# Kernel tuning notes

Measured on AMD Instinct MI355X. Metric: run time of the kernel, lower is better.

## Reference

```python
import jax, jax.numpy as jnp
import numpy as np

D_PAIR, C, N_HEAD = 128, 32, 4
HC = N_HEAD * C

def setup_inputs() -> dict:
    key = jax.random.key(0)
    ks = jax.random.split(key, 8)
    B, N = 1, 384
    Z_raw = jax.random.normal(ks[0], (B, N, N, D_PAIR), dtype=jnp.float32)
    Z_mask = jnp.ones((B, N, N), dtype=jnp.float32)
    s = 1.0 / np.sqrt(D_PAIR)
    return {
        'Z_raw': Z_raw,
        'Z_mask': Z_mask,
        'ln_w': jnp.ones((D_PAIR,), jnp.float32),
        'ln_b': jnp.zeros((D_PAIR,), jnp.float32),
        'W_b': jax.random.uniform(ks[1], (D_PAIR, N_HEAD), jnp.float32, -s, s),
        'W_qkv': jax.random.uniform(ks[2], (D_PAIR, 3 * HC), jnp.float32, -s, s),
        'W_gate': jnp.zeros((D_PAIR, HC), jnp.float32),
        'gating_bias': jnp.ones((HC,), jnp.float32),
        'W_o': jnp.zeros((HC, D_PAIR), jnp.float32),
        'out_bias': jnp.zeros((D_PAIR,), jnp.float32),
    }

def reference(Z_raw, Z_mask, ln_w, ln_b, W_b, W_qkv, W_gate, gating_bias, W_o, out_bias):
    B, N, _, D = Z_raw.shape
    # LayerNorm over d_pair
    mu = jnp.mean(Z_raw, axis=-1, keepdims=True)
    var = jnp.var(Z_raw, axis=-1, keepdims=True)
    Z = (Z_raw - mu) * jax.lax.rsqrt(var + 1e-5) * ln_w + ln_b
    # nonbatched triangle bias: [B, h, q, k]
    bias = jnp.einsum('bqkh->bhqk', jnp.einsum('bqkd,dh->bqkh', Z, W_b))
    # qkv projection: [B, N(rows), N, 3*h*c]
    qkv = jnp.einsum('bind,de->bine', Z, W_qkv)
    q, k, v = jnp.split(qkv, 3, axis=-1)
    resh = lambda t: t.reshape(B, N, N, N_HEAD, C).transpose(0, 1, 3, 2, 4)  # [B,i,h,n,c]
    q, k, v = resh(q) * (C ** -0.5), resh(k), resh(v)
    logits = jnp.einsum('bihqc,bihkc->bihqk', q, k)
    mask_bias = (Z_mask - 1.0) * 1e9  # [B, i, k]
    logits = logits + mask_bias[:, :, None, None, :] + bias[:, None, :, :, :]
    weights = jax.nn.softmax(logits, axis=-1)
    wa = jnp.einsum('bihqk,bihkc->bihqc', weights, v)
    wa = wa.transpose(0, 1, 3, 2, 4).reshape(B, N, N, HC)
    gate = jax.nn.sigmoid(jnp.einsum('bind,de->bine', Z, W_gate) + gating_bias)
    out = jnp.einsum('bine,ed->bind', gate * wa, W_o)
    # bias_dropout_add with training=False -> plain bias + residual add
    return Z_raw + out + out_bias
```

## Files before the change

### kernel.cpp

```cpp
#include <hip/hip_runtime.h>
#include <hip/hip_bf16.h>

#define NN 384
#define DP 128
#define NHEAD 4
#define CH 32
#define HCC 128

typedef __hip_bfloat16 bf16;
typedef __bf16 bf16x8 __attribute__((ext_vector_type(8)));
typedef __bf16 bf16x4 __attribute__((ext_vector_type(4)));
typedef float floatx4 __attribute__((ext_vector_type(4)));

#define QKSTRIDE 40
#define VPSTRIDE 408
#define WSTRIDE 136

__device__ __forceinline__ float b2f(bf16 x){ return __bfloat162float(x); }
__device__ __forceinline__ bf16 f2b(float x){ return __float2bfloat16(x); }

__global__ __launch_bounds__(256) void wt_kernel(
    const float* __restrict__ Wqkv, __bf16* __restrict__ Wt)
{
  int idx = blockIdx.x * 256 + threadIdx.x;
  int d = idx / NN, col = idx - d * NN;
  Wt[col * DP + d] = (__bf16)Wqkv[idx];
}

__global__ __launch_bounds__(256) void wgo_kernel(
    const float* __restrict__ Wg, const float* __restrict__ Wo,
    __bf16* __restrict__ WgT, __bf16* __restrict__ WoT)
{
  int idx = blockIdx.x * 256 + threadIdx.x;
  int r = idx >> 7, c = idx & 127;
  WgT[idx] = (__bf16)Wg[c * 128 + r];
  WoT[idx] = (__bf16)Wo[c * 128 + r];
}

__global__ __launch_bounds__(256) void ln_bias_kernel(
    const float* __restrict__ Zr, const float* __restrict__ lnw,
    const float* __restrict__ lnb, const float* __restrict__ Wb,
    bf16* __restrict__ Zn, float* __restrict__ bias)
{
  int t = threadIdx.x;
  int grp = t >> 5, lane32 = t & 31;
  int pos = blockIdx.x * 8 + grp;
  size_t base = (size_t)pos * DP;
  const float4 x = *(const float4*)(Zr + base + lane32 * 4);
  float s  = x.x + x.y + x.z + x.w;
  float s2 = x.x*x.x + x.y*x.y + x.z*x.z + x.w*x.w;
  #pragma unroll
  for (int m = 1; m < 32; m <<= 1){ s += __shfl_xor(s, m); s2 += __shfl_xor(s2, m); }
  float mean = s * (1.0f / DP);
  float var  = s2 * (1.0f / DP) - mean * mean;
  float rstd = rsqrtf(var + 1e-5f);
  const float4 w4 = *(const float4*)(lnw + lane32 * 4);
  const float4 b4 = *(const float4*)(lnb + lane32 * 4);
  float z0 = (x.x - mean) * rstd * w4.x + b4.x;
  float z1 = (x.y - mean) * rstd * w4.y + b4.y;
  float z2 = (x.z - mean) * rstd * w4.z + b4.z;
  float z3 = (x.w - mean) * rstd * w4.w + b4.w;
  bf16x4 zb = { (__bf16)z0, (__bf16)z1, (__bf16)z2, (__bf16)z3 };
  *(bf16x4*)((__bf16*)Zn + base + lane32 * 4) = zb;
  const float4 wb0 = *(const float4*)(Wb + (lane32 * 4 + 0) * NHEAD);
  const float4 wb1 = *(const float4*)(Wb + (lane32 * 4 + 1) * NHEAD);
  const float4 wb2 = *(const float4*)(Wb + (lane32 * 4 + 2) * NHEAD);
  const float4 wb3 = *(const float4*)(Wb + (lane32 * 4 + 3) * NHEAD);
  float p0 = z0*wb0.x + z1*wb1.x + z2*wb2.x + z3*wb3.x;
  float p1 = z0*wb0.y + z1*wb1.y + z2*wb2.y + z3*wb3.y;
  float p2 = z0*wb0.z + z1*wb1.z + z2*wb2.z + z3*wb3.z;
  float p3 = z0*wb0.w + z1*wb1.w + z2*wb2.w + z3*wb3.w;
  #pragma unroll
  for (int m = 1; m < 32; m <<= 1){
    p0 += __shfl_xor(p0, m); p1 += __shfl_xor(p1, m);
    p2 += __shfl_xor(p2, m); p3 += __shfl_xor(p3, m);
  }
  if (lane32 == 0){
    bias[0 * NN * NN + pos] = p0;
    bias[1 * NN * NN + pos] = p1;
    bias[2 * NN * NN + pos] = p2;
    bias[3 * NN * NN + pos] = p3;
  }
}

__global__ __launch_bounds__(256, 1) void attn_kernel(
    const __bf16* __restrict__ Zn, const __bf16* __restrict__ Wt,
    const float* __restrict__ Zm, const float* __restrict__ bias,
    __bf16* __restrict__ wa)
{
  __shared__ __align__(16) __bf16 qs[NN * QKSTRIDE];
  __shared__ __align__(16) __bf16 ks[NN * QKSTRIDE];
  __shared__ __align__(16) __bf16 vs[CH * VPSTRIDE];
  __shared__ __align__(16) __bf16 ps[4 * 16 * VPSTRIDE];
  __shared__ float maskb[NN];

  int i = blockIdx.x >> 2;
  int h = blockIdx.x & 3;
  int t = threadIdx.x;
  int wv = t >> 6;
  int lane = t & 63;
  int m16 = lane & 15;
  int quad = lane >> 4;

  for (int k = t; k < NN; k += 256)
    maskb[k] = (Zm[(size_t)i * NN + k] - 1.0f) * 1e9f;

  const float qscale = 0.17677669529663687f;

  for (int mt = wv * 6; mt < wv * 6 + 6; mt++){
    bf16x8 afr[4];
    const __bf16* arow = Zn + (size_t)(i * NN + mt * 16 + m16) * DP + quad * 8;
    #pragma unroll
    for (int kc = 0; kc < 4; kc++) afr[kc] = *(const bf16x8*)(arow + kc * 32);
    for (int nt = 0; nt < 6; nt++){
      int mat = nt >> 1;
      int colbase = mat * HCC + h * CH + (nt & 1) * 16;
      const __bf16* brow = Wt + (size_t)(colbase + m16) * DP + quad * 8;
      floatx4 acc = {0.f, 0.f, 0.f, 0.f};
      #pragma unroll
      for (int kc = 0; kc < 4; kc++){
        bf16x8 bfr = *(const bf16x8*)(brow + kc * 32);
        acc = __builtin_amdgcn_mfma_f32_16x16x32_bf16(afr[kc], bfr, acc, 0, 0, 0);
      }
      int ccol = (nt & 1) * 16 + m16;
      #pragma unroll
      for (int reg = 0; reg < 4; reg++){
        int row = mt * 16 + quad * 4 + reg;
        float v = acc[reg];
        if (mat == 0)      qs[row * QKSTRIDE + ccol] = (__bf16)(v * qscale);
        else if (mat == 1) ks[row * QKSTRIDE + ccol] = (__bf16)v;
        else               vs[ccol * VPSTRIDE + row] = (__bf16)v;
      }
    }
  }
  __syncthreads();

  const float* brow_base = bias + (size_t)h * NN * NN;
  __bf16* pw = ps + wv * 16 * VPSTRIDE;

  for (int s = 0; s < 6; s++){
    int strip = wv * 6 + s;
    bf16x8 qf = *(const bf16x8*)(qs + (strip * 16 + m16) * QKSTRIDE + quad * 8);
    floatx4 sacc[24];
    #pragma unroll
    for (int kt = 0; kt < 24; kt++){
      bf16x8 kf = *(const bf16x8*)(ks + (kt * 16 + m16) * QKSTRIDE + quad * 8);
      floatx4 z = {0.f, 0.f, 0.f, 0.f};
      sacc[kt] = __builtin_amdgcn_mfma_f32_16x16x32_bf16(qf, kf, z, 0, 0, 0);
    }
    float mx[4] = {-1e30f, -1e30f, -1e30f, -1e30f};
    #pragma unroll
    for (int kt = 0; kt < 24; kt++){
      int col = kt * 16 + m16;
      float mb = maskb[col];
      #pragma unroll
      for (int reg = 0; reg < 4; reg++){
        int row = strip * 16 + quad * 4 + reg;
        float v = sacc[kt][reg] + brow_base[(size_t)row * NN + col] + mb;
        sacc[kt][reg] = v;
        mx[reg] = fmaxf(mx[reg], v);
      }
    }
    #pragma unroll
    for (int reg = 0; reg < 4; reg++)
      for (int msk = 1; msk < 16; msk <<= 1)
        mx[reg] = fmaxf(mx[reg], __shfl_xor(mx[reg], msk));
    float sm[4] = {0.f, 0.f, 0.f, 0.f};
    #pragma unroll
    for (int kt = 0; kt < 24; kt++){
      int col = kt * 16 + m16;
      #pragma unroll
      for (int reg = 0; reg < 4; reg++){
        float p = __expf(sacc[kt][reg] - mx[reg]);
        sm[reg] += p;
        pw[(quad * 4 + reg) * VPSTRIDE + col] = (__bf16)p;
      }
    }
    #pragma unroll
    for (int reg = 0; reg < 4; reg++)
      for (int msk = 1; msk < 16; msk <<= 1)
        sm[reg] += __shfl_xor(sm[reg], msk);
    float inv[4];
    #pragma unroll
    for (int reg = 0; reg < 4; reg++) inv[reg] = 1.0f / sm[reg];

    floatx4 oacc[2] = {{0.f,0.f,0.f,0.f},{0.f,0.f,0.f,0.f}};
    #pragma unroll
    for (int kc = 0; kc < 12; kc++){
      bf16x8 pa = *(const bf16x8*)(pw + m16 * VPSTRIDE + kc * 32 + quad * 8);
      #pragma unroll
      for (int ct = 0; ct < 2; ct++){
        bf16x8 vb = *(const bf16x8*)(vs + (ct * 16 + m16) * VPSTRIDE + kc * 32 + quad * 8);
        oacc[ct] = __builtin_amdgcn_mfma_f32_16x16x32_bf16(pa, vb, oacc[ct], 0, 0, 0);
      }
    }
    #pragma unroll
    for (int ct = 0; ct < 2; ct++){
      #pragma unroll
      for (int reg = 0; reg < 4; reg++){
        int row = strip * 16 + quad * 4 + reg;
        wa[(size_t)(i * NN + row) * HCC + h * CH + ct * 16 + m16] =
            (__bf16)(oacc[ct][reg] * inv[reg]);
      }
    }
  }
}

__global__ __launch_bounds__(256, 1) void out_kernel(
    const float* __restrict__ Zr, const __bf16* __restrict__ Zn,
    const __bf16* __restrict__ wa, const __bf16* __restrict__ WgT,
    const float* __restrict__ gb, const __bf16* __restrict__ WoT,
    const float* __restrict__ ob, float* __restrict__ out)
{
  __shared__ __align__(16) __bf16 wgs[128 * WSTRIDE];
  __shared__ __align__(16) __bf16 wos[128 * WSTRIDE];
  __shared__ __align__(16) __bf16 gsh[4][16 * WSTRIDE];
  __shared__ float gbs[HCC], obs[DP];

  int t = threadIdx.x;
  int wv = t >> 6, lane = t & 63;
  int m16 = lane & 15, quad = lane >> 4;

  for (int idx = t * 8; idx < 128 * 128; idx += 256 * 8){
    int r = idx >> 7, c = idx & 127;
    *(bf16x8*)(wgs + r * WSTRIDE + c) = *(const bf16x8*)(WgT + idx);
    *(bf16x8*)(wos + r * WSTRIDE + c) = *(const bf16x8*)(WoT + idx);
  }
  if (t < 128){ gbs[t] = gb[t]; obs[t] = ob[t]; }
  __syncthreads();

  int mbase = blockIdx.x * 128;
  __bf16* gstrip = gsh[wv];

  for (int sp = 0; sp < 2; sp++){
    int row0 = mbase + (sp * 4 + wv) * 16;
    bf16x8 afr[4];
    const __bf16* arow = Zn + (size_t)(row0 + m16) * DP + quad * 8;
    #pragma unroll
    for (int kc = 0; kc < 4; kc++) afr[kc] = *(const bf16x8*)(arow + kc * 32);
    #pragma unroll
    for (int nt = 0; nt < 8; nt++){
      floatx4 acc = {0.f, 0.f, 0.f, 0.f};
      #pragma unroll
      for (int kc = 0; kc < 4; kc++){
        bf16x8 bfr = *(const bf16x8*)(wgs + (nt * 16 + m16) * WSTRIDE + kc * 32 + quad * 8);
        acc = __builtin_amdgcn_mfma_f32_16x16x32_bf16(afr[kc], bfr, acc, 0, 0, 0);
      }
      int col = nt * 16 + m16;
      #pragma unroll
      for (int reg = 0; reg < 4; reg++){
        int row = row0 + quad * 4 + reg;
        float g = 1.0f / (1.0f + __expf(-(acc[reg] + gbs[col])));
        float w = __bfloat162float(wa[(size_t)row * HCC + col]);
        gstrip[(quad * 4 + reg) * WSTRIDE + col] = (__bf16)(g * w);
      }
    }
    bf16x8 gfr[4];
    #pragma unroll
    for (int kc = 0; kc < 4; kc++)
      gfr[kc] = *(const bf16x8*)(gstrip + m16 * WSTRIDE + kc * 32 + quad * 8);
    #pragma unroll
    for (int nt = 0; nt < 8; nt++){
      floatx4 acc = {0.f, 0.f, 0.f, 0.f};
      #pragma unroll
      for (int kc = 0; kc < 4; kc++){
        bf16x8 bfr = *(const bf16x8*)(wos + (nt * 16 + m16) * WSTRIDE + kc * 32 + quad * 8);
        acc = __builtin_amdgcn_mfma_f32_16x16x32_bf16(gfr[kc], bfr, acc, 0, 0, 0);
      }
      int col = nt * 16 + m16;
      #pragma unroll
      for (int reg = 0; reg < 4; reg++){
        int row = row0 + quad * 4 + reg;
        size_t off = (size_t)row * DP + col;
        out[off] = Zr[off] + acc[reg] + obs[col];
      }
    }
  }
}

extern "C" void kernel_launch(void* const* d_in, const int* in_sizes, int n_in,
                              void* d_out, int out_size, void* d_ws, size_t ws_size,
                              hipStream_t stream)
{
  const float* Zr   = (const float*)d_in[0];
  const float* Zm   = (const float*)d_in[1];
  const float* lnw  = (const float*)d_in[2];
  const float* lnb  = (const float*)d_in[3];
  const float* Wb   = (const float*)d_in[4];
  const float* Wqkv = (const float*)d_in[5];
  const float* Wg   = (const float*)d_in[6];
  const float* gb   = (const float*)d_in[7];
  const float* Wo   = (const float*)d_in[8];
  const float* ob   = (const float*)d_in[9];
  float* out = (float*)d_out;

  char* ws = (char*)d_ws;
  size_t off = 0;
  bf16*   Zn   = (bf16*)(ws + off);           off += (size_t)NN * NN * DP * 2;
  float*  bias = (float*)(ws + off);          off += (size_t)NHEAD * NN * NN * 4;
  bf16*   wa   = (bf16*)(ws + off);           off += (size_t)NN * NN * HCC * 2;
  __bf16* Wt   = (__bf16*)(ws + off);         off += (size_t)3 * HCC * DP * 2;
  __bf16* WgT  = (__bf16*)(ws + off);         off += (size_t)DP * HCC * 2;
  __bf16* WoT  = (__bf16*)(ws + off);         off += (size_t)HCC * DP * 2;

  wt_kernel<<<(3 * HCC * DP) / 256, 256, 0, stream>>>(Wqkv, Wt);
  wgo_kernel<<<(DP * HCC) / 256, 256, 0, stream>>>(Wg, Wo, WgT, WoT);
  ln_bias_kernel<<<NN * NN / 8, 256, 0, stream>>>(Zr, lnw, lnb, Wb, Zn, bias);
  attn_kernel<<<NN * NHEAD, 256, 0, stream>>>((const __bf16*)Zn, Wt, Zm, bias, (__bf16*)wa);
  out_kernel<<<NN * NN / 128, 256, 0, stream>>>(Zr, (const __bf16*)Zn, (const __bf16*)wa,
                                                WgT, gb, WoT, ob, out);
}
```

Baseline: 493.5 us.

## Split QKV projection into a separate GEMM kernel and stream Q/K/V from global

Moves the per-row QKV projection out of the attention kernel into a dedicated qkv_gemm kernel. That kernel loads Z once per row-block for all heads and writes Q, K and a transposed V to global workspace. The query scale is folded into the weight transpose. The attention kernel now reads Q/K/V from global, seeds the MFMA accumulator with bias plus mask, and uses a transposed MFMA layout for lane-local softmax reductions and vectorized stores. It drops the large Q/K/V shared buffers to allow two blocks per CU, at the cost of extra global traffic for the Q/K/V intermediates.

```diff
diff --git a/kernel.cpp b/kernel.cpp
--- a/kernel.cpp
+++ b/kernel.cpp
@@ -12,9 +12,8 @@
 typedef __bf16 bf16x4 __attribute__((ext_vector_type(4)));
 typedef float floatx4 __attribute__((ext_vector_type(4)));
 
-#define QKSTRIDE 40
-#define VPSTRIDE 408
 #define WSTRIDE 136
+#define PSTR 392
 
 __device__ __forceinline__ float b2f(bf16 x){ return __bfloat162float(x); }
 __device__ __forceinline__ bf16 f2b(float x){ return __float2bfloat16(x); }
@@ -22,9 +21,12 @@
 __global__ __launch_bounds__(256) void wt_kernel(
     const float* __restrict__ Wqkv, __bf16* __restrict__ Wt)
 {
+  const float qscale = 0.17677669529663687f;
   int idx = blockIdx.x * 256 + threadIdx.x;
   int d = idx / NN, col = idx - d * NN;
-  Wt[col * DP + d] = (__bf16)Wqkv[idx];
+  float v = Wqkv[idx];
+  if (col < HCC) v *= qscale;
+  Wt[col * DP + d] = (__bf16)v;
 }
 
 __global__ __launch_bounds__(256) void wgo_kernel(
@@ -83,125 +85,129 @@
   }
 }
 
-__global__ __launch_bounds__(256, 1) void attn_kernel(
+__global__ __launch_bounds__(256) void qkv_gemm(
     const __bf16* __restrict__ Zn, const __bf16* __restrict__ Wt,
-    const float* __restrict__ Zm, const float* __restrict__ bias,
-    __bf16* __restrict__ wa)
-{
-  __shared__ __align__(16) __bf16 qs[NN * QKSTRIDE];
-  __shared__ __align__(16) __bf16 ks[NN * QKSTRIDE];
-  __shared__ __align__(16) __bf16 vs[CH * VPSTRIDE];
-  __shared__ __align__(16) __bf16 ps[4 * 16 * VPSTRIDE];
-  __shared__ float maskb[NN];
+    __bf16* __restrict__ q_g, __bf16* __restrict__ k_g, __bf16* __restrict__ v_g)
+{
+  int i = blockIdx.x >> 1;
+  int half = blockIdx.x & 1;
+  int t = threadIdx.x;
+  int wv = t >> 6, lane = t & 63;
+  int m16 = lane & 15, quad = lane >> 4;
+
+  int mrow0 = half * 192 + wv * 48;
+
+  bf16x8 zf[3][4];
+  #pragma unroll
+  for (int mt = 0; mt < 3; mt++){
+    const __bf16* zrow = Zn + (size_t)(i * NN + mrow0 + mt * 16 + m16) * DP + quad * 8;
+    #pragma unroll
+    for (int kc = 0; kc < 4; kc++) zf[mt][kc] = *(const bf16x8*)(zrow + kc * 32);
+  }
+
+  for (int nt = 0; nt < 24; nt++){
+    bf16x8 wf[4];
+    const __bf16* wrow = Wt + (size_t)(nt * 16 + m16) * DP + quad * 8;
+    #pragma unroll
+    for (int kc = 0; kc < 4; kc++) wf[kc] = *(const bf16x8*)(wrow + kc * 32);
+    #pragma unroll
+    for (int mt = 0; mt < 3; mt++){
+      floatx4 acc = {0.f, 0.f, 0.f, 0.f};
+      if (nt < 16){
+        #pragma unroll
+        for (int kc = 0; kc < 4; kc++)
+          acc = __builtin_amdgcn_mfma_f32_16x16x32_bf16(wf[kc], zf[mt][kc], acc, 0, 0, 0);
+        bf16x4 pk = { (__bf16)acc[0], (__bf16)acc[1], (__bf16)acc[2], (__bf16)acc[3] };
+        int row = i * NN + mrow0 + mt * 16 + m16;
+        if (nt < 8)
+          *(bf16x4*)(q_g + (size_t)row * HCC + nt * 16 + quad * 4) = pk;
+        else
+          *(bf16x4*)(k_g + (size_t)row * HCC + (nt - 8) * 16 + quad * 4) = pk;
+      } else {
+        #pragma unroll
+        for (int kc = 0; kc < 4; kc++)
+          acc = __builtin_amdgcn_mfma_f32_16x16x32_bf16(zf[mt][kc], wf[kc], acc, 0, 0, 0);
+        bf16x4 pk = { (__bf16)acc[0], (__bf16)acc[1], (__bf16)acc[2], (__bf16)acc[3] };
+        int c = (nt - 16) * 16 + m16;
+        *(bf16x4*)(v_g + ((size_t)i * HCC + c) * NN + mrow0 + mt * 16 + quad * 4) = pk;
+      }
+    }
+  }
+}
+
+__global__ __launch_bounds__(256, 2) void attn_kernel(
+    const __bf16* __restrict__ q_g, const __bf16* __restrict__ k_g,
+    const __bf16* __restrict__ v_g, const float* __restrict__ Zm,
+    const float* __restrict__ bias, __bf16* __restrict__ wa)
+{
+  __shared__ __align__(16) __bf16 ps[4 * 16 * PSTR];
+  __shared__ __align__(16) float maskb[NN];
 
   int i = blockIdx.x >> 2;
   int h = blockIdx.x & 3;
   int t = threadIdx.x;
-  int wv = t >> 6;
-  int lane = t & 63;
-  int m16 = lane & 15;
-  int quad = lane >> 4;
+  int wv = t >> 6, lane = t & 63;
+  int m16 = lane & 15, quad = lane >> 4;
 
   for (int k = t; k < NN; k += 256)
     maskb[k] = (Zm[(size_t)i * NN + k] - 1.0f) * 1e9f;
-
-  const float qscale = 0.17677669529663687f;
-
-  for (int mt = wv * 6; mt < wv * 6 + 6; mt++){
-    bf16x8 afr[4];
-    const __bf16* arow = Zn + (size_t)(i * NN + mt * 16 + m16) * DP + quad * 8;
-    #pragma unroll
-    for (int kc = 0; kc < 4; kc++) afr[kc] = *(const bf16x8*)(arow + kc * 32);
-    for (int nt = 0; nt < 6; nt++){
-      int mat = nt >> 1;
-      int colbase = mat * HCC + h * CH + (nt & 1) * 16;
-      const __bf16* brow = Wt + (size_t)(colbase + m16) * DP + quad * 8;
-      floatx4 acc = {0.f, 0.f, 0.f, 0.f};
-      #pragma unroll
-      for (int kc = 0; kc < 4; kc++){
-        bf16x8 bfr = *(const bf16x8*)(brow + kc * 32);
-        acc = __builtin_amdgcn_mfma_f32_16x16x32_bf16(afr[kc], bfr, acc, 0, 0, 0);
-      }
-      int ccol = (nt & 1) * 16 + m16;
-      #pragma unroll
-      for (int reg = 0; reg < 4; reg++){
-        int row = mt * 16 + quad * 4 + reg;
-        float v = acc[reg];
-        if (mat == 0)      qs[row * QKSTRIDE + ccol] = (__bf16)(v * qscale);
-        else if (mat == 1) ks[row * QKSTRIDE + ccol] = (__bf16)v;
-        else               vs[ccol * VPSTRIDE + row] = (__bf16)v;
-      }
-    }
-  }
   __syncthreads();
 
-  const float* brow_base = bias + (size_t)h * NN * NN;
-  __bf16* pw = ps + wv * 16 * VPSTRIDE;
+  __bf16* pw = ps + wv * 16 * PSTR;
+  const float* bh = bias + (size_t)h * NN * NN;
 
   for (int s = 0; s < 6; s++){
     int strip = wv * 6 + s;
-    bf16x8 qf = *(const bf16x8*)(qs + (strip * 16 + m16) * QKSTRIDE + quad * 8);
+    int qrow = strip * 16 + m16;
+    bf16x8 qf = *(const bf16x8*)(q_g + (size_t)(i * NN + qrow) * HCC + h * CH + quad * 8);
     floatx4 sacc[24];
     #pragma unroll
     for (int kt = 0; kt < 24; kt++){
-      bf16x8 kf = *(const bf16x8*)(ks + (kt * 16 + m16) * QKSTRIDE + quad * 8);
-      floatx4 z = {0.f, 0.f, 0.f, 0.f};
-      sacc[kt] = __builtin_amdgcn_mfma_f32_16x16x32_bf16(qf, kf, z, 0, 0, 0);
-    }
-    float mx[4] = {-1e30f, -1e30f, -1e30f, -1e30f};
+      int k0 = kt * 16 + quad * 4;
+      floatx4 cin = *(const floatx4*)(bh + (size_t)qrow * NN + k0);
+      floatx4 mk  = *(const floatx4*)(maskb + k0);
+      cin += mk;
+      bf16x8 kf = *(const bf16x8*)(k_g + (size_t)(i * NN + kt * 16 + m16) * HCC + h * CH + quad * 8);
+      sacc[kt] = __builtin_amdgcn_mfma_f32_16x16x32_bf16(kf, qf, cin, 0, 0, 0);
+    }
+    float mx = -1e30f;
     #pragma unroll
     for (int kt = 0; kt < 24; kt++){
-      int col = kt * 16 + m16;
-      float mb = maskb[col];
-      #pragma unroll
-      for (int reg = 0; reg < 4; reg++){
-        int row = strip * 16 + quad * 4 + reg;
-        float v = sacc[kt][reg] + brow_base[(size_t)row * NN + col] + mb;
-        sacc[kt][reg] = v;
-        mx[reg] = fmaxf(mx[reg], v);
-      }
-    }
-    #pragma unroll
-    for (int reg = 0; reg < 4; reg++)
-      for (int msk = 1; msk < 16; msk <<= 1)
-        mx[reg] = fmaxf(mx[reg], __shfl_xor(mx[reg], msk));
-    float sm[4] = {0.f, 0.f, 0.f, 0.f};
+      mx = fmaxf(mx, fmaxf(fmaxf(sacc[kt][0], sacc[kt][1]),
+                           fmaxf(sacc[kt][2], sacc[kt][3])));
+    }
+    mx = fmaxf(mx, __shfl_xor(mx, 16));
+    mx = fmaxf(mx, __shfl_xor(mx, 32));
+    float sm = 0.f;
     #pragma unroll
     for (int kt = 0; kt < 24; kt++){
-      int col = kt * 16 + m16;
-      #pragma unroll
-      for (int reg = 0; reg < 4; reg++){
-        float p = __expf(sacc[kt][reg] - mx[reg]);
-        sm[reg] += p;
-        pw[(quad * 4 + reg) * VPSTRIDE + col] = (__bf16)p;
-      }
-    }
-    #pragma unroll
-    for (int reg = 0; reg < 4; reg++)
-      for (int msk = 1; msk < 16; msk <<= 1)
-        sm[reg] += __shfl_xor(sm[reg], msk);
-    float inv[4];
-    #pragma unroll
-    for (int reg = 0; reg < 4; reg++) inv[reg] = 1.0f / sm[reg];
-
+      float p0 = __expf(sacc[kt][0] - mx);
+      float p1 = __expf(sacc[kt][1] - mx);
+      float p2 = __expf(sacc[kt][2] - mx);
+      float p3 = __expf(sacc[kt][3] - mx);
+      sm += (p0 + p1) + (p2 + p3);
+      bf16x4 pk = { (__bf16)p0, (__bf16)p1, (__bf16)p2, (__bf16)p3 };
+      *(bf16x4*)(pw + m16 * PSTR + kt * 16 + quad * 4) = pk;
+    }
+    sm += __shfl_xor(sm, 16);
+    sm += __shfl_xor(sm, 32);
+    float inv = 1.0f / sm;
     floatx4 oacc[2] = {{0.f,0.f,0.f,0.f},{0.f,0.f,0.f,0.f}};
     #pragma unroll
     for (int kc = 0; kc < 12; kc++){
-      bf16x8 pa = *(const bf16x8*)(pw + m16 * VPSTRIDE + kc * 32 + quad * 8);
+      bf16x8 pa = *(const bf16x8*)(pw + m16 * PSTR + kc * 32 + quad * 8);
       #pragma unroll
       for (int ct = 0; ct < 2; ct++){
-        bf16x8 vb = *(const bf16x8*)(vs + (ct * 16 + m16) * VPSTRIDE + kc * 32 + quad * 8);
-        oacc[ct] = __builtin_amdgcn_mfma_f32_16x16x32_bf16(pa, vb, oacc[ct], 0, 0, 0);
+        bf16x8 vb = *(const bf16x8*)(v_g + ((size_t)i * HCC + h * CH + ct * 16 + m16) * NN
+                                          + kc * 32 + quad * 8);
+        oacc[ct] = __builtin_amdgcn_mfma_f32_16x16x32_bf16(vb, pa, oacc[ct], 0, 0, 0);
       }
     }
     #pragma unroll
     for (int ct = 0; ct < 2; ct++){
-      #pragma unroll
-      for (int reg = 0; reg < 4; reg++){
-        int row = strip * 16 + quad * 4 + reg;
-        wa[(size_t)(i * NN + row) * HCC + h * CH + ct * 16 + m16] =
-            (__bf16)(oacc[ct][reg] * inv[reg]);
-      }
+      bf16x4 pk = { (__bf16)(oacc[ct][0] * inv), (__bf16)(oacc[ct][1] * inv),
+                    (__bf16)(oacc[ct][2] * inv), (__bf16)(oacc[ct][3] * inv) };
+      *(bf16x4*)(wa + (size_t)(i * NN + qrow) * HCC + h * CH + ct * 16 + quad * 4) = pk;
     }
   }
 }
@@ -296,17 +302,21 @@
 
   char* ws = (char*)d_ws;
   size_t off = 0;
-  bf16*   Zn   = (bf16*)(ws + off);           off += (size_t)NN * NN * DP * 2;
-  float*  bias = (float*)(ws + off);          off += (size_t)NHEAD * NN * NN * 4;
-  bf16*   wa   = (bf16*)(ws + off);           off += (size_t)NN * NN * HCC * 2;
-  __bf16* Wt   = (__bf16*)(ws + off);         off += (size_t)3 * HCC * DP * 2;
-  __bf16* WgT  = (__bf16*)(ws + off);         off += (size_t)DP * HCC * 2;
-  __bf16* WoT  = (__bf16*)(ws + off);         off += (size_t)HCC * DP * 2;
+  bf16*   Zn   = (bf16*)(ws + off);    off += (size_t)NN * NN * DP * 2;
+  float*  bias = (float*)(ws + off);   off += (size_t)NHEAD * NN * NN * 4;
+  bf16*   wa   = (bf16*)(ws + off);    off += (size_t)NN * NN * HCC * 2;
+  __bf16* Wt   = (__bf16*)(ws + off);  off += (size_t)3 * HCC * DP * 2;
+  __bf16* WgT  = (__bf16*)(ws + off);  off += (size_t)DP * HCC * 2;
+  __bf16* WoT  = (__bf16*)(ws + off);  off += (size_t)HCC * DP * 2;
+  __bf16* q_g  = (__bf16*)(ws + off);  off += (size_t)NN * NN * HCC * 2;
+  __bf16* k_g  = (__bf16*)(ws + off);  off += (size_t)NN * NN * HCC * 2;
+  __bf16* v_g  = (__bf16*)(ws + off);  off += (size_t)NN * HCC * NN * 2;
 
   wt_kernel<<<(3 * HCC * DP) / 256, 256, 0, stream>>>(Wqkv, Wt);
   wgo_kernel<<<(DP * HCC) / 256, 256, 0, stream>>>(Wg, Wo, WgT, WoT);
   ln_bias_kernel<<<NN * NN / 8, 256, 0, stream>>>(Zr, lnw, lnb, Wb, Zn, bias);
-  attn_kernel<<<NN * NHEAD, 256, 0, stream>>>((const __bf16*)Zn, Wt, Zm, bias, (__bf16*)wa);
+  qkv_gemm<<<NN * 2, 256, 0, stream>>>((const __bf16*)Zn, Wt, q_g, k_g, v_g);
+  attn_kernel<<<NN * NHEAD, 256, 0, stream>>>(q_g, k_g, v_g, Zm, bias, (__bf16*)wa);
   out_kernel<<<NN * NN / 128, 256, 0, stream>>>(Zr, (const __bf16*)Zn, (const __bf16*)wa,
                                                 WgT, gb, WoT, ob, out);
 }
```

New measurement: 824.7 us. 1.67x slower.
